# Optimization experiments

Measured on AMD Instinct MI355X. Metric: run time of the kernel, lower is better.

Reference implementation:

```python
import jax, jax.numpy as jnp
import numpy as np

B, T, C, H = 8, 2048, 384, 64

def setup_inputs() -> dict:
    key = jax.random.key(0)
    k1, k2, k3, k4 = jax.random.split(key, 4)
    x = jax.random.normal(k1, (B, T, C), dtype=jnp.float32)
    Wq = jax.random.normal(k2, (C, H), dtype=jnp.float32) * (C ** -0.5)
    Wk = jax.random.normal(k3, (C, H), dtype=jnp.float32) * (C ** -0.5)
    Wv = jax.random.normal(k4, (C, H), dtype=jnp.float32) * (C ** -0.5)
    return {"x": x, "Wq": Wq, "Wk": Wk, "Wv": Wv}

def reference(x, Wq, Wk, Wv):
    # x: (B, T, C); projections: (B, T, H)
    Bn, Tn, Cn = x.shape
    q = jnp.einsum('btc,ch->bth', x, Wq)
    k = jnp.einsum('btc,ch->bth', x, Wk)
    v = jnp.einsum('btc,ch->bth', x, Wv)
    # NOTE: source scales by C**-0.5 (embedding dim), not head_size**-0.5
    weights = jnp.einsum('bth,bsh->bts', q, k) * (Cn ** -0.5)  # (B, T, T)
    causal = jnp.tril(jnp.ones((Tn, Tn), dtype=bool))
    weights = jnp.where(causal, weights, -jnp.inf)
    # NOTE: source applies softmax over dim=1 (query/row axis), reproduced faithfully
    weights = jax.nn.softmax(weights, axis=1)
    # dropout omitted (eval-mode reference)
    return jnp.einsum('bts,bsh->bth', weights, v)
```

## Files before the change

### kernel.cpp

```cpp
#include <hip/hip_runtime.h>
#include <hip/hip_bf16.h>
#include <math.h>

#define Bn 8
#define Tn 2048
#define Cn 384
#define Hn 64
#define SCALE2 0.07362241f

using bf16x8 = __attribute__((ext_vector_type(8))) short;
using f32x4  = __attribute__((ext_vector_type(4))) float;
using u32x4  = __attribute__((ext_vector_type(4))) unsigned;

#define MFMA(a, b, c) __builtin_amdgcn_mfma_f32_16x16x32_bf16((a), (b), (c), 0, 0, 0)

static __device__ __forceinline__ short f2bf(float f) {
  unsigned u = __float_as_uint(f);
  u += 0x7fffu + ((u >> 16) & 1u);
  return (short)(u >> 16);
}
static __device__ __forceinline__ float bf2f(short s) {
  return __uint_as_float(((unsigned)(unsigned short)s) << 16);
}
static __device__ __forceinline__ float fexp2(float x) {
#if __has_builtin(__builtin_amdgcn_exp2f)
  return __builtin_amdgcn_exp2f(x);
#else
  return exp2f(x);
#endif
}
static __device__ __forceinline__ unsigned pack2(float lo, float hi) {
  return (unsigned)(unsigned short)f2bf(lo) | ((unsigned)(unsigned short)f2bf(hi) << 16);
}

__global__ __launch_bounds__(256) void wconv_kernel(
    const float* __restrict__ Wq, const float* __restrict__ Wk,
    const float* __restrict__ Wv, short* __restrict__ WbT) {
  int idx = blockIdx.x * 256 + threadIdx.x;
  int n = idx / 384, k = idx - n * 384;
  const float* W = (n < 64) ? Wq : (n < 128) ? Wk : Wv;
  WbT[idx] = f2bf(W[k * 64 + (n & 63)]);
}

__global__ __launch_bounds__(256) void proj_kernel(
    const float* __restrict__ x, const short* __restrict__ WbT,
    short* __restrict__ qb, short* __restrict__ kb, short* __restrict__ vT) {
  __shared__ short xs[16][392];
  __shared__ short vtile[64][20];
  const int tid = threadIdx.x;
  const int t0 = blockIdx.x * 16;
  const float* xb = x + (size_t)t0 * Cn;
  #pragma unroll
  for (int i = 0; i < 6; ++i) {
    int j = tid + i * 256;
    int row = j / 96, colv = (j - row * 96) * 4;
    float4 v = *(const float4*)(xb + row * Cn + colv);
    short4 s4; s4.x = f2bf(v.x); s4.y = f2bf(v.y); s4.z = f2bf(v.z); s4.w = f2bf(v.w);
    *(short4*)(&xs[row][colv]) = s4;
  }
  __syncthreads();
  const int w = tid >> 6, l15 = tid & 15, quad = (tid & 63) >> 4;
  f32x4 acc[3] = {};
  for (int ks = 0; ks < 12; ++ks) {
    bf16x8 a = *(const bf16x8*)(&xs[l15][ks * 32 + quad * 8]);
    #pragma unroll
    for (int cf = 0; cf < 3; ++cf) {
      bf16x8 bfr = *(const bf16x8*)(WbT + (size_t)(48 * w + 16 * cf + l15) * Cn + ks * 32 + quad * 8);
      acc[cf] = MFMA(a, bfr, acc[cf]);
    }
  }
  #pragma unroll
  for (int cf = 0; cf < 3; ++cf) {
    int cbase = 48 * w + 16 * cf, c = cbase + l15;
    #pragma unroll
    for (int r = 0; r < 4; ++r) {
      int row = t0 + quad * 4 + r;
      short val = f2bf(acc[cf][r]);
      if (cbase < 64)       qb[(size_t)row * Hn + c] = val;
      else if (cbase < 128) kb[(size_t)row * Hn + (c - 64)] = val;
      else                  vtile[c - 128][quad * 4 + r] = val;
    }
  }
  __syncthreads();
  const int b = t0 >> 11, t0l = t0 & 2047;
  int h = tid >> 2, tseg = (tid & 3) * 4;
  *(short4*)(vT + ((size_t)(b * Hn + h)) * Tn + t0l + tseg) =
      *(const short4*)(&vtile[h][tseg]);
}

__global__ __launch_bounds__(256) void colstats_kernel(
    const short* __restrict__ qb, const short* __restrict__ kb,
    float* __restrict__ pL) {
  const int unit = blockIdx.x;
  const int b = unit >> 7, rem = unit & 127;
  const int j = rem >> 3, u = rem & 7;
  const int lo = (u * 33) >> 3, hi = ((u + 1) * 33) >> 3;
  const int big = 32 - j;
  const int tid = threadIdx.x, w = tid >> 6, l15 = tid & 15, quad = (tid & 63) >> 4;
  __shared__ float redl[64][17];

  auto run = [&](const int i, const int k0, const int k1, const int slot) {
    const int s0 = i << 6;
    float l[4] = {0.f, 0.f, 0.f, 0.f};
    const int n = k1 - k0;
    if (n > 0) {
      bf16x8 bk[8];
      #pragma unroll
      for (int nf = 0; nf < 4; ++nf) {
        const size_t krow = (size_t)(b * Tn + s0 + 16 * nf + l15) * Hn;
        bk[2 * nf]     = *(const bf16x8*)(kb + krow + quad * 8);
        bk[2 * nf + 1] = *(const bf16x8*)(kb + krow + 32 + quad * 8);
      }
      auto cload = [&](bf16x8& A0, bf16x8& A1, int k) {
        size_t ar = (size_t)(b * Tn + ((i + k) << 6) + 16 * w + l15) * Hn;
        A0 = *(const bf16x8*)(qb + ar + quad * 8);
        A1 = *(const bf16x8*)(qb + ar + 32 + quad * 8);
      };
      auto ccomp = [&](bf16x8 A0, bf16x8 A1, int k) {
        f32x4 sc[4] = {};
        #pragma unroll
        for (int nf = 0; nf < 4; ++nf) {
          sc[nf] = MFMA(A0, bk[2 * nf], sc[nf]);
          sc[nf] = MFMA(A1, bk[2 * nf + 1], sc[nf]);
        }
        const bool diag = (k == 0);
        const int tb = ((i + k) << 6) + 16 * w + quad * 4;
        #pragma unroll
        for (int nf = 0; nf < 4; ++nf) {
          int s = s0 + 16 * nf + l15;
          #pragma unroll
          for (int r = 0; r < 4; ++r) {
            float v = sc[nf][r] * SCALE2;
            if (diag && (tb + r) < s) v = -INFINITY;
            l[nf] += fexp2(v);
          }
        }
      };
      bf16x8 a0A, a1A, a0B, a1B, a0C, a1C;
      cload(a0A, a1A, k0);
      if (n > 1) cload(a0B, a1B, k0 + 1);
      if (n > 2) cload(a0C, a1C, k0 + 2);
      int k = k0;
      while (k + 3 < k1) {
        ccomp(a0A, a1A, k);     cload(a0A, a1A, k + 3);
        ccomp(a0B, a1B, k + 1); if (k + 4 < k1) cload(a0B, a1B, k + 4);
        ccomp(a0C, a1C, k + 2); if (k + 5 < k1) cload(a0C, a1C, k + 5);
        k += 3;
      }
      const int rem2 = k1 - k;
      if (rem2 > 0) ccomp(a0A, a1A, k);
      if (rem2 > 1) ccomp(a0B, a1B, k + 1);
      if (rem2 > 2) ccomp(a0C, a1C, k + 2);
    }
    __syncthreads();
    #pragma unroll
    for (int nf = 0; nf < 4; ++nf) redl[16 * nf + l15][w * 4 + quad] = l[nf];
    __syncthreads();
    if (tid < 64) {
      float ls = 0.f;
      #pragma unroll
      for (int q2 = 0; q2 < 16; ++q2) ls += redl[tid][q2];
      pL[unit * 128 + slot * 64 + tid] = ls;
    }
  };
  run(j, lo, min(hi, big), 0);
  run(31 - j, max(lo, big) - big, hi - big, 1);
}

__global__ __launch_bounds__(256) void vhat_kernel(
    const short* __restrict__ vT, const float* __restrict__ pL,
    short* __restrict__ vS) {
  int gid = blockIdx.x * 256 + threadIdx.x;
  size_t base = (size_t)gid * 8;
  int b = (int)(base >> 17), s = (int)(base & 2047);
  int i = s >> 6, c = s & 63;
  int j2 = (i < 16) ? i : 31 - i;
  int slot = (i < 16) ? 0 : 1;
  const float* pp = pL + (size_t)((b * 16 + j2) * 8) * 128 + slot * 64 + c;
  float L0x = 0.f, L0y = 0.f, L0z = 0.f, L0w = 0.f;
  float L1x = 0.f, L1y = 0.f, L1z = 0.f, L1w = 0.f;
  #pragma unroll
  for (int u = 0; u < 8; ++u) {
    float4 p0 = *(const float4*)(pp + u * 128);
    float4 p1 = *(const float4*)(pp + u * 128 + 4);
    L0x += p0.x; L0y += p0.y; L0z += p0.z; L0w += p0.w;
    L1x += p1.x; L1y += p1.y; L1z += p1.z; L1w += p1.w;
  }
  short4 v0 = *(const short4*)(vT + base);
  short4 v1 = *(const short4*)(vT + base + 4);
  short4 r0, r1;
  r0.x = f2bf(bf2f(v0.x) / L0x); r0.y = f2bf(bf2f(v0.y) / L0y);
  r0.z = f2bf(bf2f(v0.z) / L0z); r0.w = f2bf(bf2f(v0.w) / L0w);
  r1.x = f2bf(bf2f(v1.x) / L1x); r1.y = f2bf(bf2f(v1.y) / L1y);
  r1.z = f2bf(bf2f(v1.z) / L1z); r1.w = f2bf(bf2f(v1.w) / L1w);
  *(short4*)(vS + base) = r0;
  *(short4*)(vS + base + 4) = r1;
}

__global__ __launch_bounds__(256, 3) void outg_kernel(
    const short* __restrict__ qb, const short* __restrict__ kb,
    const short* __restrict__ vS, float* __restrict__ out) {
  const int bid = blockIdx.x;
  const int tile = 31 - (bid >> 5);
  const int sub = bid & 31;
  const int b = sub >> 2, strip = sub & 3;
  const int nch = tile + 1;
  const int tid = threadIdx.x, w = tid >> 6, l15 = tid & 15, quad = (tid & 63) >> 4;
  __shared__ unsigned plds[4][512];
  __shared__ float red[4][16][64];
  const int swz = (l15 & 7) << 4;
  int wroff[8];
  #pragma unroll
  for (int nf = 0; nf < 4; ++nf)
    #pragma unroll
    for (int p = 0; p < 2; ++p)
      wroff[2 * nf + p] = (l15 * 128 + ((nf * 32 + quad * 8 + p * 4) ^ swz)) >> 2;
  const int rd0 = (l15 * 128 + ((quad * 16) ^ swz)) >> 2;
  const int rd1 = (l15 * 128 + ((64 + quad * 16) ^ swz)) >> 2;
  const size_t QKbase = (size_t)b * Tn * Hn;
  const size_t Vbase  = (size_t)b * Hn * Tn;
  const int tbase = (tile << 6) + 16 * strip;
  const int tg = tbase + l15;

  const size_t qrow = QKbase + (size_t)(tbase + l15) * Hn;
  const bf16x8 qf0 = *(const bf16x8*)(qb + qrow + quad * 8);
  const bf16x8 qf1 = *(const bf16x8*)(qb + qrow + 32 + quad * 8);

  f32x4 acc[4] = {};
  bf16x8 kf[8], vf[8];
  auto loadK = [&](int ch) {
    const int s0 = ch << 6;
    #pragma unroll
    for (int nf = 0; nf < 4; ++nf) {
      const size_t kr = QKbase + (size_t)(s0 + 16 * nf + l15) * Hn;
      kf[2 * nf]     = *(const bf16x8*)(kb + kr + quad * 8);
      kf[2 * nf + 1] = *(const bf16x8*)(kb + kr + 32 + quad * 8);
    }
  };
  auto loadV = [&](int ch) {
    const int s0 = ch << 6;
    #pragma unroll
    for (int nf = 0; nf < 4; ++nf) {
      const size_t vr = Vbase + (size_t)(16 * nf + l15) * Tn + s0;
      vf[2 * nf]     = *(const bf16x8*)(vS + vr + quad * 8);
      vf[2 * nf + 1] = *(const bf16x8*)(vS + vr + 32 + quad * 8);
    }
  };

  if (w < nch) { loadK(w); loadV(w); }
  for (int ch = w; ch < nch; ch += 4) {
    const int s0 = ch << 6;
    f32x4 sc[4] = {};
    #pragma unroll
    for (int nf = 0; nf < 4; ++nf) {
      sc[nf] = MFMA(kf[2 * nf], qf0, sc[nf]);
      sc[nf] = MFMA(kf[2 * nf + 1], qf1, sc[nf]);
    }
    const int nx = ch + 4;
    if (nx < nch) loadK(nx);
    const bool diag = (ch == tile);
    #pragma unroll
    for (int nf = 0; nf < 4; ++nf) {
      float ev[4];
      #pragma unroll
      for (int r = 0; r < 4; ++r) {
        float v = sc[nf][r] * SCALE2;
        const int s = s0 + 16 * nf + quad * 4 + r;
        if (diag && tg < s) v = -INFINITY;
        ev[r] = fexp2(v);
      }
      plds[w][wroff[2 * nf]]     = pack2(ev[0], ev[1]);
      plds[w][wroff[2 * nf + 1]] = pack2(ev[2], ev[3]);
    }
    __asm__ __volatile__("" ::: "memory");
    const bf16x8 a0 = __builtin_bit_cast(bf16x8, *(const u32x4*)(&plds[w][rd0]));
    const bf16x8 a1 = __builtin_bit_cast(bf16x8, *(const u32x4*)(&plds[w][rd1]));
    #pragma unroll
    for (int nf = 0; nf < 4; ++nf) {
      acc[nf] = MFMA(a0, vf[2 * nf], acc[nf]);
      acc[nf] = MFMA(a1, vf[2 * nf + 1], acc[nf]);
    }
    if (nx < nch) loadV(nx);
  }

  #pragma unroll
  for (int nf = 0; nf < 4; ++nf)
    #pragma unroll
    for (int r = 0; r < 4; ++r)
      red[w][quad * 4 + r][16 * nf + l15] = acc[nf][r];
  __syncthreads();
  {
    const int row = tid >> 4, c4 = (tid & 15) * 4;
    float4 s0 = *(const float4*)(&red[0][row][c4]);
    float4 s1 = *(const float4*)(&red[1][row][c4]);
    float4 s2 = *(const float4*)(&red[2][row][c4]);
    float4 s3 = *(const float4*)(&red[3][row][c4]);
    float4 t;
    t.x = (s0.x + s1.x) + (s2.x + s3.x);
    t.y = (s0.y + s1.y) + (s2.y + s3.y);
    t.z = (s0.z + s1.z) + (s2.z + s3.z);
    t.w = (s0.w + s1.w) + (s2.w + s3.w);
    *(float4*)(&out[QKbase + (size_t)(tbase + row) * Hn + c4]) = t;
  }
}

extern "C" void kernel_launch(void* const* d_in, const int* in_sizes, int n_in,
                              void* d_out, int out_size, void* d_ws, size_t ws_size,
                              hipStream_t stream) {
  const float* x  = (const float*)d_in[0];
  const float* Wq = (const float*)d_in[1];
  const float* Wk = (const float*)d_in[2];
  const float* Wv = (const float*)d_in[3];
  char* ws = (char*)d_ws;
  short* qb   = (short*)(ws);
  short* kb   = (short*)(ws + 2097152);
  short* vT   = (short*)(ws + 4194304);
  short* vS   = (short*)(ws + 6291456);
  short* WbT  = (short*)(ws + 8388608);
  float* pL   = (float*)(ws + 8536064);
  float* outp = (float*)d_out;

  hipLaunchKernelGGL(wconv_kernel, dim3(288), dim3(256), 0, stream, Wq, Wk, Wv, WbT);
  hipLaunchKernelGGL(proj_kernel, dim3(Bn * Tn / 16), dim3(256), 0, stream, x, WbT, qb, kb, vT);
  hipLaunchKernelGGL(colstats_kernel, dim3(1024), dim3(256), 0, stream, qb, kb, pL);
  hipLaunchKernelGGL(vhat_kernel, dim3(512), dim3(256), 0, stream, vT, pL, vS);
  hipLaunchKernelGGL(outg_kernel, dim3(1024), dim3(256), 0, stream, qb, kb, vS, outp);
}
```

Before: 147.5 us.

## Process two 16-row query strips per block to reuse K/V fragments

The output kernel now handles 32 query rows per block instead of 16, so each K and V fragment loaded from global memory feeds two strips of MFMAs. The grid is halved and launch bounds drop to 2 blocks per SIMD to make room for the extra registers and the larger reduction buffer. MFMA sections are wrapped in s_setprio to favour matrix issue. The cost is fewer blocks for the triangular workload and more register pressure, with the two strips serialised through the shared P buffer.

```diff
diff --git a/kernel.cpp b/kernel.cpp
--- a/kernel.cpp
+++ b/kernel.cpp
@@ -31,6 +31,10 @@
 }
 static __device__ __forceinline__ unsigned pack2(float lo, float hi) {
   return (unsigned)(unsigned short)f2bf(lo) | ((unsigned)(unsigned short)f2bf(hi) << 16);
+}
+static __device__ __forceinline__ bf16x8 ldp(const unsigned* p) {
+  u32x4 t; t[0] = p[0]; t[1] = p[1]; t[2] = p[2]; t[3] = p[3];
+  return __builtin_bit_cast(bf16x8, t);
 }
 
 __global__ __launch_bounds__(256) void wconv_kernel(
@@ -197,17 +201,17 @@
   *(short4*)(vS + base + 4) = r1;
 }
 
-__global__ __launch_bounds__(256, 3) void outg_kernel(
+__global__ __launch_bounds__(256, 2) void outg_kernel(
     const short* __restrict__ qb, const short* __restrict__ kb,
     const short* __restrict__ vS, float* __restrict__ out) {
   const int bid = blockIdx.x;
-  const int tile = 31 - (bid >> 5);
-  const int sub = bid & 31;
-  const int b = sub >> 2, strip = sub & 3;
+  const int tile = 31 - (bid >> 4);
+  const int sub = bid & 15;
+  const int b = sub >> 1, half = sub & 1;
   const int nch = tile + 1;
   const int tid = threadIdx.x, w = tid >> 6, l15 = tid & 15, quad = (tid & 63) >> 4;
   __shared__ unsigned plds[4][512];
-  __shared__ float red[4][16][64];
+  __shared__ float red[4][32][64];
   const int swz = (l15 & 7) << 4;
   int wroff[8];
   #pragma unroll
@@ -219,14 +223,18 @@
   const int rd1 = (l15 * 128 + ((64 + quad * 16) ^ swz)) >> 2;
   const size_t QKbase = (size_t)b * Tn * Hn;
   const size_t Vbase  = (size_t)b * Hn * Tn;
-  const int tbase = (tile << 6) + 16 * strip;
-  const int tg = tbase + l15;
-
-  const size_t qrow = QKbase + (size_t)(tbase + l15) * Hn;
-  const bf16x8 qf0 = *(const bf16x8*)(qb + qrow + quad * 8);
-  const bf16x8 qf1 = *(const bf16x8*)(qb + qrow + 32 + quad * 8);
-
-  f32x4 acc[4] = {};
+  const int tbase = (tile << 6) + (half << 5);
+  const int tg0 = tbase + l15;
+  const int tg1 = tbase + 16 + l15;
+
+  const size_t qrow0 = QKbase + (size_t)(tbase + l15) * Hn;
+  const size_t qrow1 = qrow0 + 16 * Hn;
+  const bf16x8 qf00 = *(const bf16x8*)(qb + qrow0 + quad * 8);
+  const bf16x8 qf01 = *(const bf16x8*)(qb + qrow0 + 32 + quad * 8);
+  const bf16x8 qf10 = *(const bf16x8*)(qb + qrow1 + quad * 8);
+  const bf16x8 qf11 = *(const bf16x8*)(qb + qrow1 + 32 + quad * 8);
+
+  f32x4 acc0[4] = {}, acc1[4] = {};
   bf16x8 kf[8], vf[8];
   auto loadK = [&](int ch) {
     const int s0 = ch << 6;
@@ -246,19 +254,7 @@
       vf[2 * nf + 1] = *(const bf16x8*)(vS + vr + 32 + quad * 8);
     }
   };
-
-  if (w < nch) { loadK(w); loadV(w); }
-  for (int ch = w; ch < nch; ch += 4) {
-    const int s0 = ch << 6;
-    f32x4 sc[4] = {};
-    #pragma unroll
-    for (int nf = 0; nf < 4; ++nf) {
-      sc[nf] = MFMA(kf[2 * nf], qf0, sc[nf]);
-      sc[nf] = MFMA(kf[2 * nf + 1], qf1, sc[nf]);
-    }
-    const int nx = ch + 4;
-    if (nx < nch) loadK(nx);
-    const bool diag = (ch == tile);
+  auto strip = [&](const f32x4 (&sc)[4], int s0, bool diag, int tg, f32x4 (&acc)[4]) {
     #pragma unroll
     for (int nf = 0; nf < 4; ++nf) {
       float ev[4];
@@ -272,35 +268,62 @@
       plds[w][wroff[2 * nf]]     = pack2(ev[0], ev[1]);
       plds[w][wroff[2 * nf + 1]] = pack2(ev[2], ev[3]);
     }
-    __asm__ __volatile__("" ::: "memory");
-    const bf16x8 a0 = __builtin_bit_cast(bf16x8, *(const u32x4*)(&plds[w][rd0]));
-    const bf16x8 a1 = __builtin_bit_cast(bf16x8, *(const u32x4*)(&plds[w][rd1]));
+    const bf16x8 a0 = ldp(&plds[w][rd0]);
+    const bf16x8 a1 = ldp(&plds[w][rd1]);
+    __builtin_amdgcn_s_setprio(1);
     #pragma unroll
     for (int nf = 0; nf < 4; ++nf) {
       acc[nf] = MFMA(a0, vf[2 * nf], acc[nf]);
       acc[nf] = MFMA(a1, vf[2 * nf + 1], acc[nf]);
     }
+    __builtin_amdgcn_s_setprio(0);
+  };
+
+  if (w < nch) { loadK(w); loadV(w); }
+  for (int ch = w; ch < nch; ch += 4) {
+    const int s0 = ch << 6;
+    f32x4 sc0[4] = {}, sc1[4] = {};
+    __builtin_amdgcn_s_setprio(1);
+    #pragma unroll
+    for (int nf = 0; nf < 4; ++nf) {
+      sc0[nf] = MFMA(kf[2 * nf], qf00, sc0[nf]);
+      sc0[nf] = MFMA(kf[2 * nf + 1], qf01, sc0[nf]);
+    }
+    #pragma unroll
+    for (int nf = 0; nf < 4; ++nf) {
+      sc1[nf] = MFMA(kf[2 * nf], qf10, sc1[nf]);
+      sc1[nf] = MFMA(kf[2 * nf + 1], qf11, sc1[nf]);
+    }
+    __builtin_amdgcn_s_setprio(0);
+    const int nx = ch + 4;
+    if (nx < nch) loadK(nx);
+    const bool diag = (ch == tile);
+    strip(sc0, s0, diag, tg0, acc0);
+    strip(sc1, s0, diag, tg1, acc1);
     if (nx < nch) loadV(nx);
   }
 
   #pragma unroll
   for (int nf = 0; nf < 4; ++nf)
     #pragma unroll
-    for (int r = 0; r < 4; ++r)
-      red[w][quad * 4 + r][16 * nf + l15] = acc[nf][r];
+    for (int r = 0; r < 4; ++r) {
+      red[w][quad * 4 + r][16 * nf + l15]      = acc0[nf][r];
+      red[w][16 + quad * 4 + r][16 * nf + l15] = acc1[nf][r];
+    }
   __syncthreads();
   {
-    const int row = tid >> 4, c4 = (tid & 15) * 4;
-    float4 s0 = *(const float4*)(&red[0][row][c4]);
-    float4 s1 = *(const float4*)(&red[1][row][c4]);
-    float4 s2 = *(const float4*)(&red[2][row][c4]);
-    float4 s3 = *(const float4*)(&red[3][row][c4]);
-    float4 t;
-    t.x = (s0.x + s1.x) + (s2.x + s3.x);
-    t.y = (s0.y + s1.y) + (s2.y + s3.y);
-    t.z = (s0.z + s1.z) + (s2.z + s3.z);
-    t.w = (s0.w + s1.w) + (s2.w + s3.w);
-    *(float4*)(&out[QKbase + (size_t)(tbase + row) * Hn + c4]) = t;
+    const int row = tid >> 3, c8 = (tid & 7) * 8;
+    float4 t0 = {0.f, 0.f, 0.f, 0.f}, t1 = {0.f, 0.f, 0.f, 0.f};
+    #pragma unroll
+    for (int ww = 0; ww < 4; ++ww) {
+      float4 s0 = *(const float4*)(&red[ww][row][c8]);
+      float4 s1 = *(const float4*)(&red[ww][row][c8 + 4]);
+      t0.x += s0.x; t0.y += s0.y; t0.z += s0.z; t0.w += s0.w;
+      t1.x += s1.x; t1.y += s1.y; t1.z += s1.z; t1.w += s1.w;
+    }
+    float* o = &out[QKbase + (size_t)(tbase + row) * Hn + c8];
+    *(float4*)(o) = t0;
+    *(float4*)(o + 4) = t1;
   }
 }
 
@@ -324,5 +347,5 @@
   hipLaunchKernelGGL(proj_kernel, dim3(Bn * Tn / 16), dim3(256), 0, stream, x, WbT, qb, kb, vT);
   hipLaunchKernelGGL(colstats_kernel, dim3(1024), dim3(256), 0, stream, qb, kb, pL);
   hipLaunchKernelGGL(vhat_kernel, dim3(512), dim3(256), 0, stream, vT, pL, vS);
-  hipLaunchKernelGGL(outg_kernel, dim3(1024), dim3(256), 0, stream, qb, kb, vS, outp);
-}
+  hipLaunchKernelGGL(outg_kernel, dim3(512), dim3(256), 0, stream, qb, kb, vS, outp);
+}
```

After: 137.5 us. 1.07x faster.

## Drop vhat pass: atomic column sums, fold 1/L into outg, prescale Wq

Applied to the files above, without the earlier changes.

Removes the vhat kernel and the scaled-V buffer. colstats now splits work into twice as many blocks and atomically accumulates column sums into a zeroed Lsum buffer. outg loads reciprocal column sums into LDS and multiplies each exp term by them before the PV MFMA. The softmax scale is folded into Wq during weight conversion, and s_setprio wraps the MFMA blocks. The occupancy hint and the colstats prefetch depth change as well. Atomics make the summation order nondeterministic, and the per-block LDS reciprocal table adds work to every outg block.

```diff
diff --git a/kernel.cpp b/kernel.cpp
--- a/kernel.cpp
+++ b/kernel.cpp
@@ -18,9 +18,6 @@
   unsigned u = __float_as_uint(f);
   u += 0x7fffu + ((u >> 16) & 1u);
   return (short)(u >> 16);
-}
-static __device__ __forceinline__ float bf2f(short s) {
-  return __uint_as_float(((unsigned)(unsigned short)s) << 16);
 }
 static __device__ __forceinline__ float fexp2(float x) {
 #if __has_builtin(__builtin_amdgcn_exp2f)
@@ -29,17 +26,32 @@
   return exp2f(x);
 #endif
 }
+static __device__ __forceinline__ float frcp(float x) {
+#if __has_builtin(__builtin_amdgcn_rcpf)
+  return __builtin_amdgcn_rcpf(x);
+#else
+  return 1.0f / x;
+#endif
+}
 static __device__ __forceinline__ unsigned pack2(float lo, float hi) {
   return (unsigned)(unsigned short)f2bf(lo) | ((unsigned)(unsigned short)f2bf(hi) << 16);
 }
+static __device__ __forceinline__ bf16x8 ldp(const unsigned* p) {
+  u32x4 t; t[0] = p[0]; t[1] = p[1]; t[2] = p[2]; t[3] = p[3];
+  return __builtin_bit_cast(bf16x8, t);
+}
 
 __global__ __launch_bounds__(256) void wconv_kernel(
     const float* __restrict__ Wq, const float* __restrict__ Wk,
-    const float* __restrict__ Wv, short* __restrict__ WbT) {
+    const float* __restrict__ Wv, short* __restrict__ WbT,
+    float* __restrict__ Lsum) {
   int idx = blockIdx.x * 256 + threadIdx.x;
+  if (idx < Bn * Tn) Lsum[idx] = 0.f;
   int n = idx / 384, k = idx - n * 384;
   const float* W = (n < 64) ? Wq : (n < 128) ? Wk : Wv;
-  WbT[idx] = f2bf(W[k * 64 + (n & 63)]);
+  float wv = W[k * 64 + (n & 63)];
+  if (n < 64) wv *= SCALE2;
+  WbT[idx] = f2bf(wv);
 }
 
 __global__ __launch_bounds__(256) void proj_kernel(
@@ -88,18 +100,19 @@
       *(const short4*)(&vtile[h][tseg]);
 }
 
-__global__ __launch_bounds__(256) void colstats_kernel(
+__global__ __launch_bounds__(256, 4) void colstats_kernel(
     const short* __restrict__ qb, const short* __restrict__ kb,
-    float* __restrict__ pL) {
-  const int unit = blockIdx.x;
-  const int b = unit >> 7, rem = unit & 127;
-  const int j = rem >> 3, u = rem & 7;
-  const int lo = (u * 33) >> 3, hi = ((u + 1) * 33) >> 3;
+    float* __restrict__ Lsum) {
+  const int bid = blockIdx.x;
+  const int b = bid & 7;
+  const int rem = bid >> 3;
+  const int j = rem >> 4, u = rem & 15;
+  const int lo = (u * 33) >> 4, hi = ((u + 1) * 33) >> 4;
   const int big = 32 - j;
   const int tid = threadIdx.x, w = tid >> 6, l15 = tid & 15, quad = (tid & 63) >> 4;
   __shared__ float redl[64][17];
 
-  auto run = [&](const int i, const int k0, const int k1, const int slot) {
+  auto run = [&](const int i, const int k0, const int k1) {
     const int s0 = i << 6;
     float l[4] = {0.f, 0.f, 0.f, 0.f};
     const int n = k1 - k0;
@@ -118,11 +131,13 @@
       };
       auto ccomp = [&](bf16x8 A0, bf16x8 A1, int k) {
         f32x4 sc[4] = {};
+        __builtin_amdgcn_s_setprio(1);
         #pragma unroll
         for (int nf = 0; nf < 4; ++nf) {
           sc[nf] = MFMA(A0, bk[2 * nf], sc[nf]);
           sc[nf] = MFMA(A1, bk[2 * nf + 1], sc[nf]);
         }
+        __builtin_amdgcn_s_setprio(0);
         const bool diag = (k == 0);
         const int tb = ((i + k) << 6) + 16 * w + quad * 4;
         #pragma unroll
@@ -130,27 +145,23 @@
           int s = s0 + 16 * nf + l15;
           #pragma unroll
           for (int r = 0; r < 4; ++r) {
-            float v = sc[nf][r] * SCALE2;
+            float v = sc[nf][r];
             if (diag && (tb + r) < s) v = -INFINITY;
             l[nf] += fexp2(v);
           }
         }
       };
-      bf16x8 a0A, a1A, a0B, a1B, a0C, a1C;
+      bf16x8 a0A, a1A, a0B, a1B;
       cload(a0A, a1A, k0);
       if (n > 1) cload(a0B, a1B, k0 + 1);
-      if (n > 2) cload(a0C, a1C, k0 + 2);
       int k = k0;
-      while (k + 3 < k1) {
-        ccomp(a0A, a1A, k);     cload(a0A, a1A, k + 3);
-        ccomp(a0B, a1B, k + 1); if (k + 4 < k1) cload(a0B, a1B, k + 4);
-        ccomp(a0C, a1C, k + 2); if (k + 5 < k1) cload(a0C, a1C, k + 5);
-        k += 3;
+      while (k + 2 < k1) {
+        ccomp(a0A, a1A, k);     cload(a0A, a1A, k + 2);
+        ccomp(a0B, a1B, k + 1); if (k + 3 < k1) cload(a0B, a1B, k + 3);
+        k += 2;
       }
-      const int rem2 = k1 - k;
-      if (rem2 > 0) ccomp(a0A, a1A, k);
-      if (rem2 > 1) ccomp(a0B, a1B, k + 1);
-      if (rem2 > 2) ccomp(a0C, a1C, k + 2);
+      if (k < k1)     ccomp(a0A, a1A, k);
+      if (k + 1 < k1) ccomp(a0B, a1B, k + 1);
     }
     __syncthreads();
     #pragma unroll
@@ -160,54 +171,32 @@
       float ls = 0.f;
       #pragma unroll
       for (int q2 = 0; q2 < 16; ++q2) ls += redl[tid][q2];
-      pL[unit * 128 + slot * 64 + tid] = ls;
+      atomicAdd(&Lsum[b * Tn + s0 + tid], ls);
     }
   };
-  run(j, lo, min(hi, big), 0);
-  run(31 - j, max(lo, big) - big, hi - big, 1);
-}
-
-__global__ __launch_bounds__(256) void vhat_kernel(
-    const short* __restrict__ vT, const float* __restrict__ pL,
-    short* __restrict__ vS) {
-  int gid = blockIdx.x * 256 + threadIdx.x;
-  size_t base = (size_t)gid * 8;
-  int b = (int)(base >> 17), s = (int)(base & 2047);
-  int i = s >> 6, c = s & 63;
-  int j2 = (i < 16) ? i : 31 - i;
-  int slot = (i < 16) ? 0 : 1;
-  const float* pp = pL + (size_t)((b * 16 + j2) * 8) * 128 + slot * 64 + c;
-  float L0x = 0.f, L0y = 0.f, L0z = 0.f, L0w = 0.f;
-  float L1x = 0.f, L1y = 0.f, L1z = 0.f, L1w = 0.f;
-  #pragma unroll
-  for (int u = 0; u < 8; ++u) {
-    float4 p0 = *(const float4*)(pp + u * 128);
-    float4 p1 = *(const float4*)(pp + u * 128 + 4);
-    L0x += p0.x; L0y += p0.y; L0z += p0.z; L0w += p0.w;
-    L1x += p1.x; L1y += p1.y; L1z += p1.z; L1w += p1.w;
-  }
-  short4 v0 = *(const short4*)(vT + base);
-  short4 v1 = *(const short4*)(vT + base + 4);
-  short4 r0, r1;
-  r0.x = f2bf(bf2f(v0.x) / L0x); r0.y = f2bf(bf2f(v0.y) / L0y);
-  r0.z = f2bf(bf2f(v0.z) / L0z); r0.w = f2bf(bf2f(v0.w) / L0w);
-  r1.x = f2bf(bf2f(v1.x) / L1x); r1.y = f2bf(bf2f(v1.y) / L1y);
-  r1.z = f2bf(bf2f(v1.z) / L1z); r1.w = f2bf(bf2f(v1.w) / L1w);
-  *(short4*)(vS + base) = r0;
-  *(short4*)(vS + base + 4) = r1;
-}
-
-__global__ __launch_bounds__(256, 3) void outg_kernel(
+  run(j, lo, min(hi, big));
+  run(31 - j, max(lo, big) - big, hi - big);
+}
+
+__global__ __launch_bounds__(256, 4) void outg_kernel(
     const short* __restrict__ qb, const short* __restrict__ kb,
-    const short* __restrict__ vS, float* __restrict__ out) {
+    const short* __restrict__ vT, const float* __restrict__ Lsum,
+    float* __restrict__ out) {
   const int bid = blockIdx.x;
   const int tile = 31 - (bid >> 5);
   const int sub = bid & 31;
-  const int b = sub >> 2, strip = sub & 3;
+  const int b = sub & 7, quarter = sub >> 3;
   const int nch = tile + 1;
   const int tid = threadIdx.x, w = tid >> 6, l15 = tid & 15, quad = (tid & 63) >> 4;
-  __shared__ unsigned plds[4][512];
-  __shared__ float red[4][16][64];
+  __shared__ alignas(16) unsigned plds[4][512];
+  __shared__ alignas(16) float red[4][16][64];
+  __shared__ alignas(16) float rcpl[2048];
+
+  const int smax = nch << 6;
+  for (int s = tid; s < smax; s += 256)
+    rcpl[s] = frcp(Lsum[b * Tn + s]);
+  __syncthreads();
+
   const int swz = (l15 & 7) << 4;
   int wroff[8];
   #pragma unroll
@@ -219,10 +208,10 @@
   const int rd1 = (l15 * 128 + ((64 + quad * 16) ^ swz)) >> 2;
   const size_t QKbase = (size_t)b * Tn * Hn;
   const size_t Vbase  = (size_t)b * Hn * Tn;
-  const int tbase = (tile << 6) + 16 * strip;
+  const int tbase = (tile << 6) + (quarter << 4);
   const int tg = tbase + l15;
 
-  const size_t qrow = QKbase + (size_t)(tbase + l15) * Hn;
+  const size_t qrow = QKbase + (size_t)tg * Hn;
   const bf16x8 qf0 = *(const bf16x8*)(qb + qrow + quad * 8);
   const bf16x8 qf1 = *(const bf16x8*)(qb + qrow + 32 + quad * 8);
 
@@ -242,8 +231,8 @@
     #pragma unroll
     for (int nf = 0; nf < 4; ++nf) {
       const size_t vr = Vbase + (size_t)(16 * nf + l15) * Tn + s0;
-      vf[2 * nf]     = *(const bf16x8*)(vS + vr + quad * 8);
-      vf[2 * nf + 1] = *(const bf16x8*)(vS + vr + 32 + quad * 8);
+      vf[2 * nf]     = *(const bf16x8*)(vT + vr + quad * 8);
+      vf[2 * nf + 1] = *(const bf16x8*)(vT + vr + 32 + quad * 8);
     }
   };
 
@@ -251,35 +240,39 @@
   for (int ch = w; ch < nch; ch += 4) {
     const int s0 = ch << 6;
     f32x4 sc[4] = {};
+    __builtin_amdgcn_s_setprio(1);
     #pragma unroll
     for (int nf = 0; nf < 4; ++nf) {
       sc[nf] = MFMA(kf[2 * nf], qf0, sc[nf]);
       sc[nf] = MFMA(kf[2 * nf + 1], qf1, sc[nf]);
     }
+    __builtin_amdgcn_s_setprio(0);
     const int nx = ch + 4;
     if (nx < nch) loadK(nx);
     const bool diag = (ch == tile);
     #pragma unroll
     for (int nf = 0; nf < 4; ++nf) {
-      float ev[4];
+      float4 rl4 = *(const float4*)&rcpl[s0 + 16 * nf + 4 * quad];
+      float p[4];
       #pragma unroll
       for (int r = 0; r < 4; ++r) {
-        float v = sc[nf][r] * SCALE2;
-        const int s = s0 + 16 * nf + quad * 4 + r;
+        float v = sc[nf][r];
+        const int s = s0 + 16 * nf + 4 * quad + r;
         if (diag && tg < s) v = -INFINITY;
-        ev[r] = fexp2(v);
+        p[r] = fexp2(v) * (&rl4.x)[r];
       }
-      plds[w][wroff[2 * nf]]     = pack2(ev[0], ev[1]);
-      plds[w][wroff[2 * nf + 1]] = pack2(ev[2], ev[3]);
-    }
-    __asm__ __volatile__("" ::: "memory");
-    const bf16x8 a0 = __builtin_bit_cast(bf16x8, *(const u32x4*)(&plds[w][rd0]));
-    const bf16x8 a1 = __builtin_bit_cast(bf16x8, *(const u32x4*)(&plds[w][rd1]));
+      plds[w][wroff[2 * nf]]     = pack2(p[0], p[1]);
+      plds[w][wroff[2 * nf + 1]] = pack2(p[2], p[3]);
+    }
+    const bf16x8 a0 = ldp(&plds[w][rd0]);
+    const bf16x8 a1 = ldp(&plds[w][rd1]);
+    __builtin_amdgcn_s_setprio(1);
     #pragma unroll
     for (int nf = 0; nf < 4; ++nf) {
       acc[nf] = MFMA(a0, vf[2 * nf], acc[nf]);
       acc[nf] = MFMA(a1, vf[2 * nf + 1], acc[nf]);
     }
+    __builtin_amdgcn_s_setprio(0);
     if (nx < nch) loadV(nx);
   }
 
@@ -315,14 +308,12 @@
   short* qb   = (short*)(ws);
   short* kb   = (short*)(ws + 2097152);
   short* vT   = (short*)(ws + 4194304);
-  short* vS   = (short*)(ws + 6291456);
-  short* WbT  = (short*)(ws + 8388608);
-  float* pL   = (float*)(ws + 8536064);
+  short* WbT  = (short*)(ws + 6291456);
+  float* Lsum = (float*)(ws + 6438912);
   float* outp = (float*)d_out;
 
-  hipLaunchKernelGGL(wconv_kernel, dim3(288), dim3(256), 0, stream, Wq, Wk, Wv, WbT);
+  hipLaunchKernelGGL(wconv_kernel, dim3(288), dim3(256), 0, stream, Wq, Wk, Wv, WbT, Lsum);
   hipLaunchKernelGGL(proj_kernel, dim3(Bn * Tn / 16), dim3(256), 0, stream, x, WbT, qb, kb, vT);
-  hipLaunchKernelGGL(colstats_kernel, dim3(1024), dim3(256), 0, stream, qb, kb, pL);
-  hipLaunchKernelGGL(vhat_kernel, dim3(512), dim3(256), 0, stream, vT, pL, vS);
-  hipLaunchKernelGGL(outg_kernel, dim3(1024), dim3(256), 0, stream, qb, kb, vS, outp);
-}
+  hipLaunchKernelGGL(colstats_kernel, dim3(2048), dim3(256), 0, stream, qb, kb, Lsum);
+  hipLaunchKernelGGL(outg_kernel, dim3(1024), dim3(256), 0, stream, qb, kb, vT, Lsum, outp);
+}
```

After: 151.0 us. +2.4%, slower.
